# Optimization experiments

Hardware: AMD Instinct MI355X
Metric: run time of the kernel (lower is better)

## Reference

```python
import jax, jax.numpy as jnp
import numpy as np

N_HEAD = 16
N_KV_HEAD = 4
N_EMBD = 2048

def rotate_half(x):
    x1, x2 = jnp.split(x, 2, axis=-1)
    return jnp.concatenate([-x2, x1], axis=-1)

def rope_tables(T, k):
    # angles = 10000^(-2*i/k) for i in [0, k/2); cos/sin repeated twice along last dim
    inv = jnp.power(10000.0, -2.0 * jnp.arange(k // 2, dtype=jnp.float32) / k)
    ang = jnp.arange(T, dtype=jnp.float32)[:, None] * inv[None, :]  # [T, k/2]
    cos = jnp.tile(jnp.cos(ang), (1, 2))  # [T, k]
    sin = jnp.tile(jnp.sin(ang), (1, 2))
    return cos, sin

def setup_inputs() -> dict:
    key = jax.random.key(0)
    ks = jax.random.split(key, 5)
    B, T, D = 4, 1024, N_EMBD
    g, h = N_KV_HEAD, N_HEAD
    k = D // h
    s = 0.02
    return {
        'x': jax.random.normal(ks[0], (B, T, D), dtype=jnp.float32),
        'Wq': jax.random.normal(ks[1], (D, D), dtype=jnp.float32) * s,
        'Wk': jax.random.normal(ks[2], (D, g * k), dtype=jnp.float32) * s,
        'Wv': jax.random.normal(ks[3], (D, g * k), dtype=jnp.float32) * s,
        'Wo': jax.random.normal(ks[4], (D, D), dtype=jnp.float32) * s,
    }

def reference(x, Wq, Wk, Wv, Wo):
    B, T, D = x.shape
    h, g = N_HEAD, N_KV_HEAD
    k = D // h
    Q = (x @ Wq).reshape(B, T, h, k).transpose(0, 2, 1, 3)  # [B,h,T,k]
    K = (x @ Wk).reshape(B, T, g, k).transpose(0, 2, 1, 3)  # [B,g,T,k]
    V = (x @ Wv).reshape(B, T, g, k).transpose(0, 2, 1, 3)
    # GQA: repeat_interleave kv heads to match query heads
    K = jnp.repeat(K, h // g, axis=1)  # [B,h,T,k]
    V = jnp.repeat(V, h // g, axis=1)
    cos, sin = rope_tables(T, k)
    cos = cos[None, None]  # [1,1,T,k]
    sin = sin[None, None]
    Q = Q * cos + rotate_half(Q) * sin
    K = K * cos + rotate_half(K) * sin
    scores = jnp.einsum('bhqk,bhsk->bhqs', Q, K) / jnp.sqrt(jnp.float32(k))
    causal = jnp.tril(jnp.ones((T, T), dtype=bool))
    scores = jnp.where(causal[None, None], scores, -jnp.inf)
    A = jax.nn.softmax(scores, axis=-1)
    Y = jnp.einsum('bhqs,bhsk->bhqk', A, V)
    Y = Y.transpose(0, 2, 1, 3).reshape(B, T, D)
    return Y @ Wo
```

## Files before the change

kernel.cpp:

```cpp
#include <hip/hip_runtime.h>
#include <math.h>

#define B_ 4
#define T_ 1024
#define D_ 2048
#define NH 16
#define NKV 4
#define HD 128
#define KV_D 512
#define QKV_S 2560

typedef __attribute__((ext_vector_type(8))) short short8;
typedef __attribute__((ext_vector_type(4))) float f32x4;

__device__ __forceinline__ ushort f2b(float f) {
    unsigned u = __float_as_uint(f);
    return (ushort)((u + 0x7fffu + ((u >> 16) & 1u)) >> 16);
}
__device__ __forceinline__ float b2f(ushort u) {
    return __uint_as_float((unsigned)u << 16);
}

#if __has_builtin(__builtin_amdgcn_exp2f)
#define EXP2F(x) __builtin_amdgcn_exp2f(x)
#else
#define EXP2F(x) __expf((x) * 0.6931471805599453f)
#endif

#define ASYNC_COPY16(g, l)                                                  \
    __builtin_amdgcn_global_load_lds(                                       \
        (const __attribute__((address_space(1))) void*)(g),                 \
        (__attribute__((address_space(3))) void*)(l), 16, 0, 0)

__global__ __launch_bounds__(256) void prep_all(const float* __restrict__ x,
                                                const float* __restrict__ Wq,
                                                const float* __restrict__ Wk,
                                                const float* __restrict__ Wv,
                                                const float* __restrict__ Wo,
                                                ushort* __restrict__ xb,
                                                ushort* __restrict__ WqkvT,
                                                ushort* __restrict__ WoT,
                                                float2* __restrict__ tab) {
    __shared__ float tile[32][33];
    const int bid = blockIdx.x;
    if (bid < 8192) {
        const int i = bid * 256 + threadIdx.x;
        const float4 v = ((const float4*)x)[i];
        ushort4 u;
        u.x = f2b(v.x); u.y = f2b(v.y); u.z = f2b(v.z); u.w = f2b(v.w);
        ((ushort4*)xb)[i] = u;
        return;
    }
    if (bid >= 18432) {
        const int idx = (bid - 18432) * 256 + threadIdx.x;
        const int t = idx >> 6, i = idx & 63;
        const float inv = exp2f((float)i * (-13.287712379549449f / 64.0f));
        const float ang = (float)t * inv;
        tab[idx] = make_float2(cosf(ang), sinf(ang));
        return;
    }
    const float* W;
    ushort* WT;
    int N, rb;
    if (bid < 12288)      { W = Wq; WT = WqkvT;                           N = D_;   rb = bid - 8192; }
    else if (bid < 13312) { W = Wk; WT = WqkvT + (size_t)D_ * D_;         N = KV_D; rb = bid - 12288; }
    else if (bid < 14336) { W = Wv; WT = WqkvT + (size_t)(D_+KV_D) * D_;  N = KV_D; rb = bid - 13312; }
    else                  { W = Wo; WT = WoT;                             N = D_;   rb = bid - 14336; }
    const int bxn = N / 32;
    const int n0 = (rb % bxn) * 32, k0 = (rb / bxn) * 32;
    const int tx = threadIdx.x & 31, ty = threadIdx.x >> 5;
    for (int i = ty; i < 32; i += 8)
        tile[i][tx] = W[(size_t)(k0 + i) * N + n0 + tx];
    __syncthreads();
    for (int i = ty; i < 32; i += 8)
        WT[(size_t)(n0 + i) * D_ + k0 + tx] = f2b(tile[tx][i]);
}

__global__ __launch_bounds__(256) void gemm_qkv(const ushort* __restrict__ A,
                                                const ushort* __restrict__ BT,
                                                ushort* __restrict__ QKV,
                                                ushort* __restrict__ Vt,
                                                const float2* __restrict__ tab) {
    __shared__ ushort smem[128 * 136];
    ushort* As = smem;
    ushort* Bs = smem + 4096;
    const int K = D_;
    const int tid = threadIdx.x;
    const int m0 = blockIdx.y * 128, n0 = blockIdx.x * 128;
    const int hid = n0 >> 7;
    const int wave = tid >> 6, lane = tid & 63;
    const int wm = (wave >> 1) * 64, wn = (wave & 1) * 64;
    const int lrow = lane & 15;
    const int quad = lane >> 4;

    f32x4 acc[4][4];
    const f32x4 zero = {0.f, 0.f, 0.f, 0.f};
#pragma unroll
    for (int i = 0; i < 4; ++i)
#pragma unroll
        for (int j = 0; j < 4; ++j) acc[i][j] = zero;

    const int srow = tid >> 2;
    const int scol = (tid & 3) * 8;
    const ushort* Ag = A + (size_t)(m0 + srow) * K + scol;
    const ushort* Bg = BT + (size_t)(n0 + srow) * K + scol;
    ushort* AsT = As + tid * 8;
    ushort* BsT = Bs + tid * 8;

    for (int k0 = 0; k0 < K; k0 += 32) {
        ASYNC_COPY16(Ag + k0, AsT);
        ASYNC_COPY16(Ag + k0 + (size_t)64 * K, AsT + 64 * 32);
        ASYNC_COPY16(Bg + k0, BsT);
        ASYNC_COPY16(Bg + k0 + (size_t)64 * K, BsT + 64 * 32);
        __syncthreads();

        short8 a[4], b[4];
#pragma unroll
        for (int mt = 0; mt < 4; ++mt)
            a[mt] = *(const short8*)&As[(wm + mt * 16 + lrow) * 32 + quad * 8];
#pragma unroll
        for (int nt = 0; nt < 4; ++nt)
            b[nt] = *(const short8*)&Bs[(wn + nt * 16 + lrow) * 32 + quad * 8];
#pragma unroll
        for (int mt = 0; mt < 4; ++mt)
#pragma unroll
            for (int nt = 0; nt < 4; ++nt)
                acc[mt][nt] = __builtin_amdgcn_mfma_f32_16x16x32_bf16(
                    a[mt], b[nt], acc[mt][nt], 0, 0, 0);
        __syncthreads();
    }

    ushort* Epi = smem;
#pragma unroll
    for (int mt = 0; mt < 4; ++mt)
#pragma unroll
        for (int nt = 0; nt < 4; ++nt)
#pragma unroll
            for (int r = 0; r < 4; ++r)
                Epi[(wm + mt * 16 + quad * 4 + r) * 136 + wn + nt * 16 + lrow] =
                    f2b(acc[mt][nt][r]);
    __syncthreads();

    const int b = m0 >> 10;
    const int t0 = m0 & 1023;

    if (hid < NH + NKV) {
        const bool isQ = hid < NH;
        const size_t colbase = isQ ? hid * HD : (size_t)D_ + (hid - NH) * HD;
        const float sc = isQ ? (0.08838834764831845f * 1.4426950408889634f) : 1.0f;
        const int r = tid >> 1;
        const int hf = tid & 1;
        const int t = t0 + r;
        ushort* orow = QKV + (size_t)(m0 + r) * QKV_S + colbase;
        const float4* tab4 = (const float4*)tab;
#pragma unroll
        for (int jj = 0; jj < 4; ++jj) {
            const int dbase = hf * 32 + jj * 8;
            const short8 lo = *(const short8*)&Epi[r * 136 + dbase];
            const short8 hi = *(const short8*)&Epi[r * 136 + 64 + dbase];
            ushort olo[8], ohi[8];
#pragma unroll
            for (int k = 0; k < 4; ++k) {
                const float4 cs = tab4[((t * 64 + dbase) >> 1) + k];
                const float x1a = b2f(lo[2 * k]),     x2a = b2f(hi[2 * k]);
                const float x1b = b2f(lo[2 * k + 1]), x2b = b2f(hi[2 * k + 1]);
                olo[2 * k]     = f2b((x1a * cs.x - x2a * cs.y) * sc);
                ohi[2 * k]     = f2b((x2a * cs.x + x1a * cs.y) * sc);
                olo[2 * k + 1] = f2b((x1b * cs.z - x2b * cs.w) * sc);
                ohi[2 * k + 1] = f2b((x2b * cs.z + x1b * cs.w) * sc);
            }
            *(short8*)&orow[dbase]      = *(short8*)olo;
            *(short8*)&orow[dbase + 64] = *(short8*)ohi;
        }
    } else {
        const int kv = hid - (NH + NKV);
        const int d = tid & 127;
        const int hf = tid >> 7;
        ushort* vrow = Vt + ((size_t)((b * NKV + kv) * HD + d)) * T_ + t0 + hf * 64;
#pragma unroll
        for (int jj = 0; jj < 8; ++jj) {
            ushort pk[8];
#pragma unroll
            for (int k = 0; k < 8; ++k)
                pk[k] = Epi[(hf * 64 + jj * 8 + k) * 136 + d];
            *(short8*)&vrow[jj * 8] = *(short8*)pk;
        }
    }
}

__global__ __launch_bounds__(256) void gemm_bf16(const ushort* __restrict__ A,
                                                 const ushort* __restrict__ BT,
                                                 float* __restrict__ C,
                                                 int M, int N, int K) {
    __shared__ ushort As[128 * 32];
    __shared__ ushort Bs[128 * 32];
    const int tid = threadIdx.x;
    const int m0 = blockIdx.y * 128, n0 = blockIdx.x * 128;
    const int wave = tid >> 6, lane = tid & 63;
    const int wm = (wave >> 1) * 64, wn = (wave & 1) * 64;
    const int lrow = lane & 15;
    const int quad = lane >> 4;

    f32x4 acc[4][4];
    const f32x4 zero = {0.f, 0.f, 0.f, 0.f};
#pragma unroll
    for (int i = 0; i < 4; ++i)
#pragma unroll
        for (int j = 0; j < 4; ++j) acc[i][j] = zero;

    const int srow = tid >> 2;
    const int scol = (tid & 3) * 8;
    const ushort* Ag = A + (size_t)(m0 + srow) * K + scol;
    const ushort* Bg = BT + (size_t)(n0 + srow) * K + scol;
    ushort* AsT = As + tid * 8;
    ushort* BsT = Bs + tid * 8;

    for (int k0 = 0; k0 < K; k0 += 32) {
        ASYNC_COPY16(Ag + k0, AsT);
        ASYNC_COPY16(Ag + k0 + (size_t)64 * K, AsT + 64 * 32);
        ASYNC_COPY16(Bg + k0, BsT);
        ASYNC_COPY16(Bg + k0 + (size_t)64 * K, BsT + 64 * 32);
        __syncthreads();

        short8 a[4], b[4];
#pragma unroll
        for (int mt = 0; mt < 4; ++mt)
            a[mt] = *(const short8*)&As[(wm + mt * 16 + lrow) * 32 + quad * 8];
#pragma unroll
        for (int nt = 0; nt < 4; ++nt)
            b[nt] = *(const short8*)&Bs[(wn + nt * 16 + lrow) * 32 + quad * 8];
#pragma unroll
        for (int mt = 0; mt < 4; ++mt)
#pragma unroll
            for (int nt = 0; nt < 4; ++nt)
                acc[mt][nt] = __builtin_amdgcn_mfma_f32_16x16x32_bf16(
                    a[mt], b[nt], acc[mt][nt], 0, 0, 0);
        __syncthreads();
    }

    const int crow = quad * 4;
    const int ccol = lrow;
#pragma unroll
    for (int mt = 0; mt < 4; ++mt)
#pragma unroll
        for (int nt = 0; nt < 4; ++nt)
#pragma unroll
            for (int r = 0; r < 4; ++r)
                C[(size_t)(m0 + wm + mt * 16 + crow + r) * N +
                  n0 + wn + nt * 16 + ccol] = acc[mt][nt][r];
}

__global__ __launch_bounds__(256) void attn_mfma(const ushort* __restrict__ QKV,
                                                 const ushort* __restrict__ Vt,
                                                 ushort* __restrict__ Yb) {
    __shared__ ushort Ks[64][136];
    __shared__ ushort Vs[128][72];
    __shared__ ushort Ps[4][16][72];

    const int bh = blockIdx.x;
    const int qt = (int)gridDim.y - 1 - (int)blockIdx.y;
    const int b = bh >> 4, h = bh & 15;
    const int kvh = h >> 2;
    const int q0 = qt * 64;
    const int tid = threadIdx.x;
    const int wave = tid >> 6, lane = tid & 63;
    const int ln = lane & 15, quad = lane >> 4;

    short8 qf[4];
    {
        const ushort* qp = QKV + ((size_t)(b * T_ + q0 + wave * 16 + ln)) * QKV_S + h * HD + quad * 8;
#pragma unroll
        for (int f = 0; f < 4; ++f) qf[f] = *(const short8*)(qp + f * 32);
    }

    const size_t kv_row = (size_t)((b * NKV + kvh) * HD);
    const ushort* const Vbase = Vt + kv_row * T_;
    const ushort* const Kbase = QKV + ((size_t)(b * T_)) * QKV_S + D_ + kvh * HD;

    short8 kreg[4], vreg[4];
#define LOAD_KV(s0_)                                                        \
    do {                                                                    \
        _Pragma("unroll")                                                   \
        for (int c = 0; c < 4; ++c) {                                       \
            const int cid = tid + 256 * c;                                  \
            const int s = cid >> 4, ch = cid & 15;                          \
            kreg[c] = *(const short8*)&Kbase[((size_t)((s0_) + s)) * QKV_S + ch * 8]; \
        }                                                                   \
        _Pragma("unroll")                                                   \
        for (int c = 0; c < 4; ++c) {                                       \
            const int cid = tid + 256 * c;                                  \
            const int d = cid >> 3, ch = cid & 7;                           \
            vreg[c] = *(const short8*)&Vbase[(size_t)d * T_ + (s0_) + ch * 8]; \
        }                                                                   \
    } while (0)

    f32x4 acc[8];
    const f32x4 zero = {0.f, 0.f, 0.f, 0.f};
#pragma unroll
    for (int j = 0; j < 8; ++j) acc[j] = zero;
    float m_r[4], l_r[4];
#pragma unroll
    for (int r = 0; r < 4; ++r) { m_r[r] = -INFINITY; l_r[r] = 0.f; }

    const int qrow = q0 + wave * 16 + quad * 4;

    LOAD_KV(0);

    for (int kt = 0; kt <= qt; ++kt) {
        const int s0 = kt * 64;
        __syncthreads();
#pragma unroll
        for (int c = 0; c < 4; ++c) {
            const int cid = tid + 256 * c;
            const int s = cid >> 4, ch = cid & 15;
            *(short8*)&Ks[s][ch * 8] = kreg[c];
        }
#pragma unroll
        for (int c = 0; c < 4; ++c) {
            const int cid = tid + 256 * c;
            const int d = cid >> 3, ch = cid & 7;
            *(short8*)&Vs[d][ch * 8] = vreg[c];
        }
        __syncthreads();

        if (kt < qt) LOAD_KV(s0 + 64);

        float sc[4][4];
#pragma unroll
        for (int ct = 0; ct < 4; ++ct) {
            f32x4 s4 = zero;
#pragma unroll
            for (int f = 0; f < 4; ++f)
                s4 = __builtin_amdgcn_mfma_f32_16x16x32_bf16(
                    qf[f], *(const short8*)&Ks[ct * 16 + ln][f * 32 + quad * 8], s4, 0, 0, 0);
#pragma unroll
            for (int r = 0; r < 4; ++r) sc[ct][r] = s4[r];
        }
        if (kt == qt) {
#pragma unroll
            for (int ct = 0; ct < 4; ++ct)
#pragma unroll
                for (int r = 0; r < 4; ++r)
                    if (s0 + ct * 16 + ln > qrow + r) sc[ct][r] = -INFINITY;
        }
        float alpha[4];
#pragma unroll
        for (int r = 0; r < 4; ++r) {
            float mx = fmaxf(fmaxf(sc[0][r], sc[1][r]), fmaxf(sc[2][r], sc[3][r]));
            mx = fmaxf(mx, __shfl_xor(mx, 1));
            mx = fmaxf(mx, __shfl_xor(mx, 2));
            mx = fmaxf(mx, __shfl_xor(mx, 4));
            mx = fmaxf(mx, __shfl_xor(mx, 8));
            const float mnew = fmaxf(m_r[r], mx);
            alpha[r] = EXP2F(m_r[r] - mnew);
            m_r[r] = mnew;
#pragma unroll
            for (int ct = 0; ct < 4; ++ct) sc[ct][r] = EXP2F(sc[ct][r] - mnew);
            float sum = (sc[0][r] + sc[1][r]) + (sc[2][r] + sc[3][r]);
            sum += __shfl_xor(sum, 1);
            sum += __shfl_xor(sum, 2);
            sum += __shfl_xor(sum, 4);
            sum += __shfl_xor(sum, 8);
            l_r[r] = l_r[r] * alpha[r] + sum;
        }
#pragma unroll
        for (int ct = 0; ct < 4; ++ct)
#pragma unroll
            for (int r = 0; r < 4; ++r)
                Ps[wave][quad * 4 + r][ct * 16 + ln] = f2b(sc[ct][r]);
#pragma unroll
        for (int j = 0; j < 8; ++j)
#pragma unroll
            for (int r = 0; r < 4; ++r) acc[j][r] *= alpha[r];
        const short8 pa0 = *(const short8*)&Ps[wave][ln][quad * 8];
        const short8 pa1 = *(const short8*)&Ps[wave][ln][32 + quad * 8];
#pragma unroll
        for (int j = 0; j < 8; ++j) {
            acc[j] = __builtin_amdgcn_mfma_f32_16x16x32_bf16(
                pa0, *(const short8*)&Vs[j * 16 + ln][quad * 8], acc[j], 0, 0, 0);
            acc[j] = __builtin_amdgcn_mfma_f32_16x16x32_bf16(
                pa1, *(const short8*)&Vs[j * 16 + ln][32 + quad * 8], acc[j], 0, 0, 0);
        }
    }
#undef LOAD_KV

    float invl[4];
#pragma unroll
    for (int r = 0; r < 4; ++r) invl[r] = 1.f / l_r[r];
    ushort* yb = Yb + ((size_t)(b * T_ + qrow)) * D_ + h * HD + ln;
#pragma unroll
    for (int r = 0; r < 4; ++r)
#pragma unroll
        for (int j = 0; j < 8; ++j)
            yb[(size_t)r * D_ + j * 16] = f2b(acc[j][r] * invl[r]);
}

extern "C" void kernel_launch(void* const* d_in, const int* in_sizes, int n_in,
                              void* d_out, int out_size, void* d_ws, size_t ws_size,
                              hipStream_t stream) {
    const float* x  = (const float*)d_in[0];
    const float* Wq = (const float*)d_in[1];
    const float* Wk = (const float*)d_in[2];
    const float* Wv = (const float*)d_in[3];
    const float* Wo = (const float*)d_in[4];
    float* out = (float*)d_out;

    char* w = (char*)d_ws;
    ushort* xb    = (ushort*)w;  w += (size_t)4096 * D_ * 2;
    ushort* WqkvT = (ushort*)w;  w += (size_t)3072 * D_ * 2;
    ushort* QKV   = (ushort*)w;  w += (size_t)4096 * QKV_S * 2;
    ushort* Vt    = (ushort*)w;  w += (size_t)B_ * KV_D * T_ * 2;
    ushort* Yb    = (ushort*)w;  w += (size_t)4096 * D_ * 2;
    ushort* WoT   = (ushort*)w;  w += (size_t)D_ * D_ * 2;
    float2* tab   = (float2*)w;  w += (size_t)T_ * 64 * 8;

    const int M = B_ * T_;
    dim3 blk(256);

    prep_all<<<18688, blk, 0, stream>>>(x, Wq, Wk, Wv, Wo, xb, WqkvT, WoT, tab);

    gemm_qkv<<<dim3(3072 / 128, M / 128), blk, 0, stream>>>(xb, WqkvT, QKV, Vt, tab);

    attn_mfma<<<dim3(B_ * NH, T_ / 64), blk, 0, stream>>>(QKV, Vt, Yb);

    gemm_bf16<<<dim3(D_ / 128, M / 128), blk, 0, stream>>>(Yb, WoT, out, M, D_, D_);
}
```

Baseline: 292.9 us.

## Widen GEMM K-tile to 64 with XOR-swizzled LDS and 64x64 transpose tiles

Both bf16 GEMMs now stage a 64-wide K slice per iteration instead of 32. The LDS layout uses an XOR swizzle on the column chunk to avoid bank conflicts on the MFMA operand reads. Halving the K iterations halves the barrier count per GEMM, at the cost of twice the shared memory per block for gemm_bf16. The weight transpose in prep_all moves to 64x64 tiles with float4 loads and 16-byte stores, which cuts the block count and makes global accesses wider.

New measurement: 285.2 us. 2.6% less time.

```diff
diff --git a/kernel.cpp b/kernel.cpp
--- a/kernel.cpp
+++ b/kernel.cpp
@@ -31,6 +31,8 @@
     __builtin_amdgcn_global_load_lds(                                       \
         (const __attribute__((address_space(1))) void*)(g),                 \
         (__attribute__((address_space(3))) void*)(l), 16, 0, 0)
+
+#define MFMA16(ap, bp, cc) cc = __builtin_amdgcn_mfma_f32_16x16x32_bf16(ap, bp, cc, 0, 0, 0)
 
 __global__ __launch_bounds__(256) void prep_all(const float* __restrict__ x,
                                                 const float* __restrict__ Wq,
@@ -41,18 +43,19 @@
                                                 ushort* __restrict__ WqkvT,
                                                 ushort* __restrict__ WoT,
                                                 float2* __restrict__ tab) {
-    __shared__ float tile[32][33];
+    __shared__ float tile[64][65];
     const int bid = blockIdx.x;
+    const int tid = threadIdx.x;
     if (bid < 8192) {
-        const int i = bid * 256 + threadIdx.x;
+        const int i = bid * 256 + tid;
         const float4 v = ((const float4*)x)[i];
         ushort4 u;
         u.x = f2b(v.x); u.y = f2b(v.y); u.z = f2b(v.z); u.w = f2b(v.w);
         ((ushort4*)xb)[i] = u;
         return;
     }
-    if (bid >= 18432) {
-        const int idx = (bid - 18432) * 256 + threadIdx.x;
+    if (bid >= 10752) {
+        const int idx = (bid - 10752) * 256 + tid;
         const int t = idx >> 6, i = idx & 63;
         const float inv = exp2f((float)i * (-13.287712379549449f / 64.0f));
         const float ang = (float)t * inv;
@@ -62,18 +65,30 @@
     const float* W;
     ushort* WT;
     int N, rb;
-    if (bid < 12288)      { W = Wq; WT = WqkvT;                           N = D_;   rb = bid - 8192; }
-    else if (bid < 13312) { W = Wk; WT = WqkvT + (size_t)D_ * D_;         N = KV_D; rb = bid - 12288; }
-    else if (bid < 14336) { W = Wv; WT = WqkvT + (size_t)(D_+KV_D) * D_;  N = KV_D; rb = bid - 13312; }
-    else                  { W = Wo; WT = WoT;                             N = D_;   rb = bid - 14336; }
-    const int bxn = N / 32;
-    const int n0 = (rb % bxn) * 32, k0 = (rb / bxn) * 32;
-    const int tx = threadIdx.x & 31, ty = threadIdx.x >> 5;
-    for (int i = ty; i < 32; i += 8)
-        tile[i][tx] = W[(size_t)(k0 + i) * N + n0 + tx];
+    if (bid < 9216)      { W = Wq; WT = WqkvT;                           N = D_;   rb = bid - 8192; }
+    else if (bid < 9472) { W = Wk; WT = WqkvT + (size_t)D_ * D_;         N = KV_D; rb = bid - 9216; }
+    else if (bid < 9728) { W = Wv; WT = WqkvT + (size_t)(D_+KV_D) * D_;  N = KV_D; rb = bid - 9472; }
+    else                 { W = Wo; WT = WoT;                             N = D_;   rb = bid - 9728; }
+    const int bxn = N / 64;
+    const int n0 = (rb % bxn) * 64, k0 = (rb / bxn) * 64;
+    const int tx = tid & 15, ty = tid >> 4;
+#pragma unroll
+    for (int i = 0; i < 4; ++i) {
+        const int r = ty + i * 16;
+        const float4 v = *(const float4*)&W[(size_t)(k0 + r) * N + n0 + tx * 4];
+        tile[r][tx * 4 + 0] = v.x;
+        tile[r][tx * 4 + 1] = v.y;
+        tile[r][tx * 4 + 2] = v.z;
+        tile[r][tx * 4 + 3] = v.w;
+    }
     __syncthreads();
-    for (int i = ty; i < 32; i += 8)
-        WT[(size_t)(n0 + i) * D_ + k0 + tx] = f2b(tile[tx][i]);
+    const int n = tid >> 2, ch = (tid & 3) * 16;
+    ushort tmp[16];
+#pragma unroll
+    for (int j = 0; j < 16; ++j) tmp[j] = f2b(tile[ch + j][n]);
+    ushort* orow = WT + (size_t)(n0 + n) * D_ + k0 + ch;
+    *(short8*)&orow[0] = *(short8*)&tmp[0];
+    *(short8*)&orow[8] = *(short8*)&tmp[8];
 }
 
 __global__ __launch_bounds__(256) void gemm_qkv(const ushort* __restrict__ A,
@@ -83,7 +98,7 @@
                                                 const float2* __restrict__ tab) {
     __shared__ ushort smem[128 * 136];
     ushort* As = smem;
-    ushort* Bs = smem + 4096;
+    ushort* Bs = smem + 8192;
     const int K = D_;
     const int tid = threadIdx.x;
     const int m0 = blockIdx.y * 128, n0 = blockIdx.x * 128;
@@ -100,33 +115,38 @@
 #pragma unroll
         for (int j = 0; j < 4; ++j) acc[i][j] = zero;
 
-    const int srow = tid >> 2;
-    const int scol = (tid & 3) * 8;
+    const int srow = tid >> 3;
+    const int scol = ((tid & 7) * 8) ^ ((srow & 7) << 3);
     const ushort* Ag = A + (size_t)(m0 + srow) * K + scol;
     const ushort* Bg = BT + (size_t)(n0 + srow) * K + scol;
     ushort* AsT = As + tid * 8;
     ushort* BsT = Bs + tid * 8;
-
-    for (int k0 = 0; k0 < K; k0 += 32) {
-        ASYNC_COPY16(Ag + k0, AsT);
-        ASYNC_COPY16(Ag + k0 + (size_t)64 * K, AsT + 64 * 32);
-        ASYNC_COPY16(Bg + k0, BsT);
-        ASYNC_COPY16(Bg + k0 + (size_t)64 * K, BsT + 64 * 32);
-        __syncthreads();
-
-        short8 a[4], b[4];
-#pragma unroll
-        for (int mt = 0; mt < 4; ++mt)
-            a[mt] = *(const short8*)&As[(wm + mt * 16 + lrow) * 32 + quad * 8];
-#pragma unroll
-        for (int nt = 0; nt < 4; ++nt)
-            b[nt] = *(const short8*)&Bs[(wn + nt * 16 + lrow) * 32 + quad * 8];
-#pragma unroll
-        for (int mt = 0; mt < 4; ++mt)
+    const int swr = (lrow & 7) << 3;
+
+    for (int k0 = 0; k0 < K; k0 += 64) {
+#pragma unroll
+        for (int c = 0; c < 4; ++c) {
+            ASYNC_COPY16(Ag + k0 + (size_t)(c * 32) * K, AsT + c * 2048);
+            ASYNC_COPY16(Bg + k0 + (size_t)(c * 32) * K, BsT + c * 2048);
+        }
+        __syncthreads();
+
+#pragma unroll
+        for (int ks = 0; ks < 2; ++ks) {
+            const int col = (quad * 8) ^ (ks * 32) ^ swr;
+            short8 a[4], b[4];
+#pragma unroll
+            for (int mt = 0; mt < 4; ++mt)
+                a[mt] = *(const short8*)&As[(wm + mt * 16 + lrow) * 64 + col];
 #pragma unroll
             for (int nt = 0; nt < 4; ++nt)
-                acc[mt][nt] = __builtin_amdgcn_mfma_f32_16x16x32_bf16(
-                    a[mt], b[nt], acc[mt][nt], 0, 0, 0);
+                b[nt] = *(const short8*)&Bs[(wn + nt * 16 + lrow) * 64 + col];
+#pragma unroll
+            for (int mt = 0; mt < 4; ++mt)
+#pragma unroll
+                for (int nt = 0; nt < 4; ++nt)
+                    MFMA16(a[mt], b[nt], acc[mt][nt]);
+        }
         __syncthreads();
     }
 
@@ -192,8 +212,8 @@
                                                  const ushort* __restrict__ BT,
                                                  float* __restrict__ C,
                                                  int M, int N, int K) {
-    __shared__ ushort As[128 * 32];
-    __shared__ ushort Bs[128 * 32];
+    __shared__ ushort As[128 * 64];
+    __shared__ ushort Bs[128 * 64];
     const int tid = threadIdx.x;
     const int m0 = blockIdx.y * 128, n0 = blockIdx.x * 128;
     const int wave = tid >> 6, lane = tid & 63;
@@ -208,33 +228,38 @@
 #pragma unroll
         for (int j = 0; j < 4; ++j) acc[i][j] = zero;
 
-    const int srow = tid >> 2;
-    const int scol = (tid & 3) * 8;
+    const int srow = tid >> 3;
+    const int scol = ((tid & 7) * 8) ^ ((srow & 7) << 3);
     const ushort* Ag = A + (size_t)(m0 + srow) * K + scol;
     const ushort* Bg = BT + (size_t)(n0 + srow) * K + scol;
     ushort* AsT = As + tid * 8;
     ushort* BsT = Bs + tid * 8;
-
-    for (int k0 = 0; k0 < K; k0 += 32) {
-        ASYNC_COPY16(Ag + k0, AsT);
-        ASYNC_COPY16(Ag + k0 + (size_t)64 * K, AsT + 64 * 32);
-        ASYNC_COPY16(Bg + k0, BsT);
-        ASYNC_COPY16(Bg + k0 + (size_t)64 * K, BsT + 64 * 32);
-        __syncthreads();
-
-        short8 a[4], b[4];
-#pragma unroll
-        for (int mt = 0; mt < 4; ++mt)
-            a[mt] = *(const short8*)&As[(wm + mt * 16 + lrow) * 32 + quad * 8];
-#pragma unroll
-        for (int nt = 0; nt < 4; ++nt)
-            b[nt] = *(const short8*)&Bs[(wn + nt * 16 + lrow) * 32 + quad * 8];
-#pragma unroll
-        for (int mt = 0; mt < 4; ++mt)
+    const int swr = (lrow & 7) << 3;
+
+    for (int k0 = 0; k0 < K; k0 += 64) {
+#pragma unroll
+        for (int c = 0; c < 4; ++c) {
+            ASYNC_COPY16(Ag + k0 + (size_t)(c * 32) * K, AsT + c * 2048);
+            ASYNC_COPY16(Bg + k0 + (size_t)(c * 32) * K, BsT + c * 2048);
+        }
+        __syncthreads();
+
+#pragma unroll
+        for (int ks = 0; ks < 2; ++ks) {
+            const int col = (quad * 8) ^ (ks * 32) ^ swr;
+            short8 a[4], b[4];
+#pragma unroll
+            for (int mt = 0; mt < 4; ++mt)
+                a[mt] = *(const short8*)&As[(wm + mt * 16 + lrow) * 64 + col];
 #pragma unroll
             for (int nt = 0; nt < 4; ++nt)
-                acc[mt][nt] = __builtin_amdgcn_mfma_f32_16x16x32_bf16(
-                    a[mt], b[nt], acc[mt][nt], 0, 0, 0);
+                b[nt] = *(const short8*)&Bs[(wn + nt * 16 + lrow) * 64 + col];
+#pragma unroll
+            for (int mt = 0; mt < 4; ++mt)
+#pragma unroll
+                for (int nt = 0; nt < 4; ++nt)
+                    MFMA16(a[mt], b[nt], acc[mt][nt]);
+        }
         __syncthreads();
     }
 
@@ -417,7 +442,7 @@
     const int M = B_ * T_;
     dim3 blk(256);
 
-    prep_all<<<18688, blk, 0, stream>>>(x, Wq, Wk, Wv, Wo, xb, WqkvT, WoT, tab);
+    prep_all<<<11008, blk, 0, stream>>>(x, Wq, Wk, Wv, Wo, xb, WqkvT, WoT, tab);
 
     gemm_qkv<<<dim3(3072 / 128, M / 128), blk, 0, stream>>>(xb, WqkvT, QKV, Vt, tab);
 
```
